# Kernel tuning notes

Hardware: AMD Instinct MI355X
Metric: run time of the kernel (lower is better)

## Reference

```python
import jax, jax.numpy as jnp
import numpy as np

B, N, C = 32, 8732, 81  # batch, SSD300 anchors, COCO classes incl. background


def setup_inputs() -> dict:
    key = jax.random.key(0)
    k1, k2, k3, k4, k5 = jax.random.split(key, 5)
    ploc = jax.random.normal(k1, (B, N, 4), jnp.float32)
    plabel = jax.random.normal(k2, (B, N, C), jnp.float32)
    gloc = jax.random.normal(k3, (B, N, 4), jnp.float32)
    labels = jax.random.randint(k4, (B, N), 1, C)
    is_pos = jax.random.uniform(k5, (B, N)) < 0.02
    glabel = jnp.where(is_pos, labels, 0).astype(jnp.int32)
    return {"ploc": ploc, "plabel": plabel, "gloc": gloc, "glabel": glabel}


def _smooth_l1(x):
    ax = jnp.abs(x)
    return jnp.where(ax < 1.0, 0.5 * ax * ax, ax - 0.5)


def reference(ploc, plabel, gloc, glabel):
    num_classes = plabel.shape[-1]
    mask = glabel.reshape(-1) > 0                      # [B*N] positive anchors
    pos_num = mask.sum()

    # Localization loss: SmoothL1 summed over 4 coords, only on positives
    loss_l = _smooth_l1(ploc.reshape(-1, 4) - gloc.reshape(-1, 4)).sum(axis=1)
    loss_l = (mask.astype(loss_l.dtype) * loss_l).sum()

    # Per-anchor cross entropy over flattened batch
    logp = jax.nn.log_softmax(plabel.reshape(-1, num_classes), axis=-1)
    gt = glabel.reshape(-1)
    loss_c = -jnp.take_along_axis(logp, gt[:, None], axis=1)[:, 0]  # [B*N]

    # Hard negative mining via double argsort (rank of each anchor's CE loss)
    con_neg = jnp.where(mask, 0.0, loss_c)
    con_idx = jnp.argsort(-con_neg)        # descending sort indices
    con_rank = jnp.argsort(con_idx)        # rank of each element
    neg_num = jnp.minimum(3 * pos_num, mask.shape[0])
    neg_mask = con_rank < neg_num

    closs = (loss_c * (mask.astype(loss_c.dtype) + neg_mask.astype(loss_c.dtype))).sum()
    total_loss = loss_l + closs
    return jnp.where(pos_num > 0, total_loss / pos_num.astype(total_loss.dtype), 0.0)
```

## Files before the change

### kernel.cpp

```cpp
#include <hip/hip_runtime.h>
#include <math.h>

#define M_TOTAL (32 * 8732)
#define M4      (M_TOTAL / 4)
#define NBLK_A  (M_TOTAL / 64)
#define NBLK_S  273
#define NREP    16

#define CON_B    ((size_t)0)
#define HISTR_B  ((size_t)M_TOTAL * 4)
#define H1_B     (HISTR_B + (size_t)NREP * 2048 * 4)
#define H2_B     (H1_B + (size_t)2048 * 4)
#define G_B      (H2_B + (size_t)1024 * 4)
#define PART_B   (G_B + 128)
#define ZERO_BYTES ((size_t)NREP * 2048 * 4 + 2048 * 4 + 1024 * 4 + 128)

struct GS {
    unsigned pn;
    float    lossl;
    float    poslc;
    unsigned b0;
    unsigned k1;
    unsigned pref;
    unsigned k2;
    float    sumhi0;
    float    sumhi1;
};

__device__ __forceinline__ float smooth_l1(float d) {
    float ad = fabsf(d);
    return (ad < 1.0f) ? 0.5f * ad * ad : ad - 0.5f;
}

#define GLLDS16(gp, lp) __builtin_amdgcn_global_load_lds( \
    (__attribute__((address_space(1))) void*)(gp),        \
    (__attribute__((address_space(3))) void*)(lp), 16, 0, 0)

__device__ void selectk256(const unsigned* cnt, int nbins, unsigned k,
                           unsigned* ssum, unsigned* pbin, unsigned* pk) {
    const int t = threadIdx.x;
    const int chunk = nbins >> 8;
    if (t == 0) { *pbin = 0u; *pk = 0u; }
    unsigned tot = 0;
    for (int j = 0; j < chunk; ++j) tot += cnt[t * chunk + j];
    ssum[t] = tot;
    __syncthreads();
    for (int off = 1; off < 256; off <<= 1) {
        const unsigned val = ssum[t];
        const unsigned add = (t + off < 256) ? ssum[t + off] : 0u;
        __syncthreads();
        ssum[t] = val + add;
        __syncthreads();
    }
    const unsigned s_after = (t < 255) ? ssum[t + 1] : 0u;
    if (k > 0u && ssum[t] >= k && k > s_after) {
        unsigned cum = s_after;
        for (int j = chunk - 1; j >= 0; --j) {
            const unsigned bin = t * chunk + j;
            const unsigned nc = cum + cnt[bin];
            if (nc >= k) { *pbin = bin; *pk = k - cum; break; }
            cum = nc;
        }
    }
    __syncthreads();
}

__global__ __launch_bounds__(256) void kA(const float* __restrict__ ploc,
                                          const float* __restrict__ plabel,
                                          const float* __restrict__ gloc,
                                          const int* __restrict__ glabel,
                                          float* __restrict__ con,
                                          unsigned* __restrict__ histR,
                                          float4* __restrict__ part) {
    __shared__ __align__(16) float stage[4 * 1296];
    __shared__ unsigned lh[2048];
    __shared__ float rf[4][3];

    const int tid  = threadIdx.x;
    const int w    = tid >> 6;
    const int lane = tid & 63;
    const int g    = lane >> 2;
    const int l    = lane & 3;

    for (int i = tid; i < 2048; i += 256) lh[i] = 0u;

    const size_t wrow0 = (size_t)blockIdx.x * 64 + (size_t)w * 16;
    const char*  gsrc  = (const char*)(plabel + wrow0 * 81);
    char*        ldst  = (char*)&stage[w * 1296];
#pragma unroll
    for (int j = 0; j < 5; ++j)
        GLLDS16(gsrc + (size_t)j * 1024 + (size_t)lane * 16, ldst + j * 1024);
    if (lane < 4)
        GLLDS16(gsrc + 5120 + (size_t)lane * 16, ldst + 5120);

    const size_t row = wrow0 + g;
    const float pl = ploc[wrow0 * 4 + lane];
    const float gl = gloc[wrow0 * 4 + lane];
    int gt = 0;
    if (l == 0) gt = glabel[row];
    const int mask = gt > 0;

    float s = smooth_l1(pl - gl);
    s += __shfl_xor(s, 1);
    s += __shfl_xor(s, 2);

    __syncthreads();

    const float* rowp = &stage[w * 1296 + g * 81];
    float v[20];
    float m = -INFINITY;
#pragma unroll
    for (int j = 0; j < 20; ++j) { v[j] = rowp[j * 4 + l]; m = fmaxf(m, v[j]); }
    float v80 = 0.0f;
    if (l == 0) { v80 = rowp[80]; m = fmaxf(m, v80); }
    m = fmaxf(m, __shfl_xor(m, 1));
    m = fmaxf(m, __shfl_xor(m, 2));

    float e = 0.0f;
#pragma unroll
    for (int j = 0; j < 20; ++j) e += __expf(v[j] - m);
    if (l == 0) e += __expf(v80 - m);
    e += __shfl_xor(e, 1);
    e += __shfl_xor(e, 2);
    const float lse = m + __logf(e);

    float wl = 0.f, wc = 0.f, wp = 0.f;
    if (l == 0) {
        const float x_gt   = rowp[gt];
        const float loss_c = lse - x_gt;
        const float cn     = mask ? 0.0f : fmaxf(loss_c, 0.0f);
        con[row] = cn;
        atomicAdd(&lh[__float_as_uint(cn) >> 21], 1u);
        if (mask) { wl = s; wc = loss_c; wp = 1.0f; }
    }
#pragma unroll
    for (int off = 4; off < 64; off <<= 1) {
        wl += __shfl_xor(wl, off);
        wc += __shfl_xor(wc, off);
        wp += __shfl_xor(wp, off);
    }
    if (lane == 0) { rf[w][0] = wl; rf[w][1] = wc; rf[w][2] = wp; }
    __syncthreads();

    if (tid == 0)
        part[blockIdx.x] = make_float4(rf[0][0] + rf[1][0] + rf[2][0] + rf[3][0],
                                       rf[0][1] + rf[1][1] + rf[2][1] + rf[3][1],
                                       rf[0][2] + rf[1][2] + rf[2][2] + rf[3][2], 0.f);

    unsigned* hrep = histR + (size_t)(blockIdx.x & (NREP - 1)) * 2048;
    for (int i = tid; i < 2048; i += 256) {
        const unsigned c = lh[i];
        if (c) atomicAdd(&hrep[i], c);
    }
}

__global__ __launch_bounds__(256) void kC(const float4* __restrict__ con4,
                                          const unsigned* __restrict__ histR,
                                          const float4* __restrict__ part,
                                          unsigned* __restrict__ h1,
                                          GS* __restrict__ G) {
    __shared__ unsigned lh[2048];
    __shared__ unsigned ssum[256];
    __shared__ unsigned sbin, sk;
    __shared__ float    wred[4];
    __shared__ float    rf3[4][3];
    const int tid = threadIdx.x;

    for (int b = tid; b < 2048; b += 256) {
        unsigned c = 0;
#pragma unroll
        for (int r = 0; r < NREP; ++r) c += histR[r * 2048 + b];
        lh[b] = c;
    }
    float sl = 0.f, sc = 0.f, sp = 0.f;
    for (int p = tid; p < NBLK_A; p += 256) {
        const float4 q = part[p];
        sl += q.x; sc += q.y; sp += q.z;
    }
#pragma unroll
    for (int off = 1; off < 64; off <<= 1) {
        sl += __shfl_xor(sl, off); sc += __shfl_xor(sc, off); sp += __shfl_xor(sp, off);
    }
    if ((tid & 63) == 0) { rf3[tid >> 6][0] = sl; rf3[tid >> 6][1] = sc; rf3[tid >> 6][2] = sp; }
    __syncthreads();
    const float tsp = rf3[0][2] + rf3[1][2] + rf3[2][2] + rf3[3][2];
    const unsigned pn = (unsigned)(tsp + 0.5f);
    unsigned k0 = 3u * pn;
    if (k0 > (unsigned)M_TOTAL) k0 = (unsigned)M_TOTAL;

    selectk256(lh, 2048, k0, ssum, &sbin, &sk);
    const unsigned b0 = sbin, k1loc = sk;

    const int i = blockIdx.x * 256 + tid;
    float s = 0.f;
    if (i < M4) {
        const float4 q = con4[i];
        const float xs[4] = {q.x, q.y, q.z, q.w};
#pragma unroll
        for (int j = 0; j < 4; ++j) {
            const unsigned u  = __float_as_uint(xs[j]);
            const unsigned hi = u >> 21;
            if (hi > b0) s += xs[j];
            else if (hi == b0) atomicAdd(&h1[(u >> 10) & 0x7FFu], 1u);
        }
    }
#pragma unroll
    for (int off = 1; off < 64; off <<= 1) s += __shfl_xor(s, off);
    if ((tid & 63) == 0) wred[tid >> 6] = s;
    __syncthreads();
    if (tid == 0) {
        const float tot = wred[0] + wred[1] + wred[2] + wred[3];
        if (tot != 0.f) atomicAdd(&G->sumhi0, tot);
        if (blockIdx.x == 0) {
            G->pn = pn;
            G->lossl = rf3[0][0] + rf3[1][0] + rf3[2][0] + rf3[3][0];
            G->poslc = rf3[0][1] + rf3[1][1] + rf3[2][1] + rf3[3][1];
            G->b0 = b0; G->k1 = k1loc;
        }
    }
}

__global__ __launch_bounds__(256) void kD(const float4* __restrict__ con4,
                                          const unsigned* __restrict__ h1,
                                          unsigned* __restrict__ h2,
                                          GS* __restrict__ G) {
    __shared__ unsigned lh[2048];
    __shared__ unsigned ssum[256];
    __shared__ unsigned sbin, sk;
    __shared__ float    wred[4];
    const int tid = threadIdx.x;

    for (int b = tid; b < 2048; b += 256) lh[b] = h1[b];
    __syncthreads();

    const unsigned b0 = G->b0;
    const unsigned k1 = G->k1;
    selectk256(lh, 2048, k1, ssum, &sbin, &sk);
    const unsigned b1 = sbin, k2loc = sk;

    const int i = blockIdx.x * 256 + tid;
    float s = 0.f;
    if (i < M4) {
        const float4 q = con4[i];
        const float xs[4] = {q.x, q.y, q.z, q.w};
#pragma unroll
        for (int j = 0; j < 4; ++j) {
            const unsigned u = __float_as_uint(xs[j]);
            if ((u >> 21) == b0) {
                const unsigned mid = (u >> 10) & 0x7FFu;
                if (mid > b1) s += xs[j];
                else if (mid == b1) atomicAdd(&h2[u & 0x3FFu], 1u);
            }
        }
    }
#pragma unroll
    for (int off = 1; off < 64; off <<= 1) s += __shfl_xor(s, off);
    if ((tid & 63) == 0) wred[tid >> 6] = s;
    __syncthreads();
    if (tid == 0) {
        const float tot = wred[0] + wred[1] + wred[2] + wred[3];
        if (tot != 0.f) atomicAdd(&G->sumhi1, tot);
        if (blockIdx.x == 0) { G->pref = (b0 << 11) | b1; G->k2 = k2loc; }
    }
}

__global__ __launch_bounds__(256) void kE(const unsigned* __restrict__ h2,
                                          const GS* __restrict__ G,
                                          float* __restrict__ out) {
    __shared__ unsigned lh[1024];
    __shared__ unsigned ssum[256];
    __shared__ unsigned sbin, sk;
    __shared__ float    wred[4];
    const int tid = threadIdx.x;

    for (int b = tid; b < 1024; b += 256) lh[b] = h2[b];
    __syncthreads();
    const unsigned pref = G->pref;
    const unsigned k2   = G->k2;
    selectk256(lh, 1024, k2, ssum, &sbin, &sk);
    const unsigned ct = sbin, r = sk;

    float s2 = 0.f;
    for (int b = tid; b < 1024; b += 256) {
        const unsigned c = lh[b];
        if ((unsigned)b > ct && c)
            s2 += (float)c * __uint_as_float((pref << 10) | (unsigned)b);
    }
#pragma unroll
    for (int off = 1; off < 64; off <<= 1) s2 += __shfl_xor(s2, off);
    if ((tid & 63) == 0) wred[tid >> 6] = s2;
    __syncthreads();

    if (tid == 0) {
        const float sumhi2 = wred[0] + wred[1] + wred[2] + wred[3];
        const unsigned pn = G->pn;
        float outv = 0.f;
        if (pn > 0u) {
            const float tval  = __uint_as_float((pref << 10) | ct);
            const float closs = G->poslc + G->sumhi0 + G->sumhi1 + sumhi2 + (float)r * tval;
            outv = (G->lossl + closs) / (float)pn;
        }
        out[0] = outv;
    }
}

extern "C" void kernel_launch(void* const* d_in, const int* in_sizes, int n_in,
                              void* d_out, int out_size, void* d_ws, size_t ws_size,
                              hipStream_t stream) {
    const float* ploc   = (const float*)d_in[0];
    const float* plabel = (const float*)d_in[1];
    const float* gloc   = (const float*)d_in[2];
    const int*   glabel = (const int*)d_in[3];
    float* out = (float*)d_out;
    char*  ws  = (char*)d_ws;

    float*    con   = (float*)(ws + CON_B);
    unsigned* histR = (unsigned*)(ws + HISTR_B);
    unsigned* h1    = (unsigned*)(ws + H1_B);
    unsigned* h2    = (unsigned*)(ws + H2_B);
    GS*       G     = (GS*)(ws + G_B);
    float4*   part  = (float4*)(ws + PART_B);

    hipMemsetAsync(ws + HISTR_B, 0, ZERO_BYTES, stream);
    kA<<<NBLK_A, 256, 0, stream>>>(ploc, plabel, gloc, glabel, con, histR, part);
    kC<<<NBLK_S, 256, 0, stream>>>((const float4*)con, histR, part, h1, G);
    kD<<<NBLK_S, 256, 0, stream>>>((const float4*)con, h1, h2, G);
    kE<<<1, 256, 0, stream>>>(h2, G, out);
}
```

Measured before the change: 174.3 us.

## Use one thread per anchor row with direct unaligned vector loads in kA

Kernel A now assigns one thread per anchor row with 256 rows per block, instead of four lanes per row with LDS staging through global_load_lds. Each thread reads its 81 logits straight from global memory as packed 4-byte-aligned float4 structs and computes max, sum-exp and lse serially, which removes the staging barrier and the cross-lane shuffles. The cost is uncoalesced strided global loads (324-byte row stride per lane), more registers per thread and fewer blocks.

```diff
diff --git a/kernel.cpp b/kernel.cpp
--- a/kernel.cpp
+++ b/kernel.cpp
@@ -3,7 +3,7 @@
 
 #define M_TOTAL (32 * 8732)
 #define M4      (M_TOTAL / 4)
-#define NBLK_A  (M_TOTAL / 64)
+#define NBLK_A  ((M_TOTAL + 255) / 256)
 #define NBLK_S  273
 #define NREP    16
 
@@ -27,14 +27,12 @@
     float    sumhi1;
 };
 
+struct __attribute__((packed, aligned(4))) f4u { float x, y, z, w; };
+
 __device__ __forceinline__ float smooth_l1(float d) {
     float ad = fabsf(d);
     return (ad < 1.0f) ? 0.5f * ad * ad : ad - 0.5f;
 }
-
-#define GLLDS16(gp, lp) __builtin_amdgcn_global_load_lds( \
-    (__attribute__((address_space(1))) void*)(gp),        \
-    (__attribute__((address_space(3))) void*)(lp), 16, 0, 0)
 
 __device__ void selectk256(const unsigned* cnt, int nbins, unsigned k,
                            unsigned* ssum, unsigned* pbin, unsigned* pk) {
@@ -72,69 +70,57 @@
                                           float* __restrict__ con,
                                           unsigned* __restrict__ histR,
                                           float4* __restrict__ part) {
-    __shared__ __align__(16) float stage[4 * 1296];
     __shared__ unsigned lh[2048];
-    __shared__ float rf[4][3];
+    __shared__ float    rf[4][3];
 
     const int tid  = threadIdx.x;
+    const int lane = tid & 63;
     const int w    = tid >> 6;
-    const int lane = tid & 63;
-    const int g    = lane >> 2;
-    const int l    = lane & 3;
+    const int row  = blockIdx.x * 256 + tid;
+    const bool live = row < M_TOTAL;
 
     for (int i = tid; i < 2048; i += 256) lh[i] = 0u;
-
-    const size_t wrow0 = (size_t)blockIdx.x * 64 + (size_t)w * 16;
-    const char*  gsrc  = (const char*)(plabel + wrow0 * 81);
-    char*        ldst  = (char*)&stage[w * 1296];
-#pragma unroll
-    for (int j = 0; j < 5; ++j)
-        GLLDS16(gsrc + (size_t)j * 1024 + (size_t)lane * 16, ldst + j * 1024);
-    if (lane < 4)
-        GLLDS16(gsrc + 5120 + (size_t)lane * 16, ldst + 5120);
-
-    const size_t row = wrow0 + g;
-    const float pl = ploc[wrow0 * 4 + lane];
-    const float gl = gloc[wrow0 * 4 + lane];
-    int gt = 0;
-    if (l == 0) gt = glabel[row];
-    const int mask = gt > 0;
-
-    float s = smooth_l1(pl - gl);
-    s += __shfl_xor(s, 1);
-    s += __shfl_xor(s, 2);
-
-    __syncthreads();
-
-    const float* rowp = &stage[w * 1296 + g * 81];
-    float v[20];
-    float m = -INFINITY;
-#pragma unroll
-    for (int j = 0; j < 20; ++j) { v[j] = rowp[j * 4 + l]; m = fmaxf(m, v[j]); }
-    float v80 = 0.0f;
-    if (l == 0) { v80 = rowp[80]; m = fmaxf(m, v80); }
-    m = fmaxf(m, __shfl_xor(m, 1));
-    m = fmaxf(m, __shfl_xor(m, 2));
-
-    float e = 0.0f;
-#pragma unroll
-    for (int j = 0; j < 20; ++j) e += __expf(v[j] - m);
-    if (l == 0) e += __expf(v80 - m);
-    e += __shfl_xor(e, 1);
-    e += __shfl_xor(e, 2);
-    const float lse = m + __logf(e);
+    __syncthreads();
 
     float wl = 0.f, wc = 0.f, wp = 0.f;
-    if (l == 0) {
-        const float x_gt   = rowp[gt];
+    if (live) {
+        const float4 pl = ((const float4*)ploc)[row];
+        const float4 gl = ((const float4*)gloc)[row];
+        const int    gt = glabel[row];
+        const int  mask = gt > 0;
+
+        const float s = smooth_l1(pl.x - gl.x) + smooth_l1(pl.y - gl.y) +
+                        smooth_l1(pl.z - gl.z) + smooth_l1(pl.w - gl.w);
+
+        const float* rb = plabel + (size_t)row * 81;
+        f4u v[20];
+#pragma unroll
+        for (int j = 0; j < 20; ++j) v[j] = ((const f4u*)rb)[j];
+        const float v80 = rb[80];
+
+        float m = v80;
+#pragma unroll
+        for (int j = 0; j < 20; ++j) {
+            m = fmaxf(m, fmaxf(fmaxf(v[j].x, v[j].y), fmaxf(v[j].z, v[j].w)));
+        }
+        float e = __expf(v80 - m);
+#pragma unroll
+        for (int j = 0; j < 20; ++j) {
+            e += __expf(v[j].x - m) + __expf(v[j].y - m) +
+                 __expf(v[j].z - m) + __expf(v[j].w - m);
+        }
+        const float lse = m + __logf(e);
+
+        const float x_gt   = rb[gt];
         const float loss_c = lse - x_gt;
         const float cn     = mask ? 0.0f : fmaxf(loss_c, 0.0f);
         con[row] = cn;
         atomicAdd(&lh[__float_as_uint(cn) >> 21], 1u);
         if (mask) { wl = s; wc = loss_c; wp = 1.0f; }
     }
-#pragma unroll
-    for (int off = 4; off < 64; off <<= 1) {
+
+#pragma unroll
+    for (int off = 1; off < 64; off <<= 1) {
         wl += __shfl_xor(wl, off);
         wc += __shfl_xor(wc, off);
         wp += __shfl_xor(wp, off);
```

After: 185.4 us. 6.3% more time.
